# Performance work log

Hardware: AMD Instinct MI355X
Metric: run time of the kernel (lower is better)

The kernel has to match this reference:

```python
import jax, jax.numpy as jnp
import numpy as np

N, E, F, H, C, G = 100000, 1000000, 64, 64, 10, 256


def setup_inputs() -> dict:
    key = jax.random.key(0)
    ks = jax.random.split(key, 16)
    s = 1.0 / np.sqrt(F)
    sh = 1.0 / np.sqrt(H)
    return {
        "x": jax.random.normal(ks[0], (N, F), dtype=jnp.float32),
        "edge_index": jax.random.randint(ks[1], (2, E), 0, N, dtype=jnp.int32),
        "edge_attr": jax.random.uniform(ks[2], (E,), dtype=jnp.float32),
        "batch": jnp.sort(jax.random.randint(ks[3], (N,), 0, G, dtype=jnp.int32)),
        "W1r": jax.random.uniform(ks[4], (F, H), minval=-s, maxval=s),
        "W1s": jax.random.uniform(ks[5], (F, H), minval=-s, maxval=s),
        "b1": jax.random.uniform(ks[6], (H,), minval=-s, maxval=s),
        "W2r": jax.random.uniform(ks[7], (H, H), minval=-sh, maxval=sh),
        "W2s": jax.random.uniform(ks[8], (H, H), minval=-sh, maxval=sh),
        "b2": jax.random.uniform(ks[9], (H,), minval=-sh, maxval=sh),
        "W3r": jax.random.uniform(ks[10], (H, H), minval=-sh, maxval=sh),
        "W3s": jax.random.uniform(ks[11], (H, H), minval=-sh, maxval=sh),
        "b3": jax.random.uniform(ks[12], (H,), minval=-sh, maxval=sh),
        "Wl": jax.random.uniform(ks[13], (H, C), minval=-sh, maxval=sh),
        "bl": jax.random.uniform(ks[14], (C,), minval=-sh, maxval=sh),
    }


def graph_conv(x, src, dst, ew, W_rel, W_root, b):
    # gather neighbor feats, weight per-edge, scatter-add to destination
    msgs = x[src] * ew[:, None]                              # [E, F]
    agg = jax.ops.segment_sum(msgs, dst, num_segments=N)     # [N, F]
    return agg @ W_rel + x @ W_root + b                      # [N, H]


def reference(x, edge_index, edge_attr, batch,
              W1r, W1s, b1, W2r, W2s, b2, W3r, W3s, b3, Wl, bl):
    src, dst = edge_index[0], edge_index[1]
    h = jax.nn.relu(graph_conv(x, src, dst, edge_attr, W1r, W1s, b1))
    h = jax.nn.relu(graph_conv(h, src, dst, edge_attr, W2r, W2s, b2))
    h = jax.nn.relu(graph_conv(h, src, dst, edge_attr, W3r, W3s, b3))
    # global mean pool over graphs in the batch
    sums = jax.ops.segment_sum(h, batch, num_segments=G)      # [G, H]
    cnts = jax.ops.segment_sum(jnp.ones((N,), h.dtype), batch, num_segments=G)
    pooled = sums / jnp.maximum(cnts, 1.0)[:, None]
    # dropout is identity in eval mode
    return pooled @ Wl + bl                                   # [G, C]
```

## Files before the change

kernel.cpp:

```cpp
#include <hip/hip_runtime.h>


#define GCN_F 64
#define GCN_C 10
#define CB_SHIFT 9
#define CB_NODES 512
#define NCB_MAX 200
#define CAP 7168
#define SC_CHUNK 2048

typedef __attribute__((ext_vector_type(8))) short bf16x8;
typedef __attribute__((ext_vector_type(4))) float f32x4;

__device__ __forceinline__ unsigned short f2b(float v) {
    union { float f; unsigned int u; } c; c.f = v;
    unsigned int u = c.u;
    return (unsigned short)((u + 0x7FFFu + ((u >> 16) & 1u)) >> 16);
}
__device__ __forceinline__ float b2f(unsigned short u) {
    union { unsigned int u; float f; } c; c.u = ((unsigned int)u) << 16; return c.f;
}

__global__ __launch_bounds__(256) void cvtz_kernel(const float* __restrict__ in,
                                                   unsigned short* __restrict__ out,
                                                   int n4, int* __restrict__ zp, int zn) {
    int gid = blockIdx.x * 256 + threadIdx.x;
    if (gid < zn) zp[gid] = 0;
    int stride = gridDim.x * 256;
    for (int i = gid; i < n4; i += stride) {
        float4 v = reinterpret_cast<const float4*>(in)[i];
        ushort4 o;
        o.x = f2b(v.x); o.y = f2b(v.y); o.z = f2b(v.z); o.w = f2b(v.w);
        reinterpret_cast<ushort4*>(out)[i] = o;
    }
}

__global__ __launch_bounds__(256) void histC_kernel(const int* __restrict__ dst,
                                                    int* __restrict__ bcnt,
                                                    int E, int NCB) {
    __shared__ int h[NCB_MAX];
    int tid = threadIdx.x;
    for (int i = tid; i < NCB; i += 256) h[i] = 0;
    __syncthreads();
    int e0 = blockIdx.x * 4096 + tid;
#pragma unroll
    for (int k = 0; k < 16; ++k) {
        int e = e0 + k * 256;
        if (e < E) atomicAdd(&h[dst[e] >> CB_SHIFT], 1);
    }
    __syncthreads();
    for (int i = tid; i < NCB; i += 256)
        if (h[i]) atomicAdd(&bcnt[i], h[i]);
}

__global__ void bscan_kernel(const int* __restrict__ bcnt, int* __restrict__ gstart,
                             int nb) {
    int lane = threadIdx.x;
    int carry = 0;
    for (int base = 0; base < nb; base += 64) {
        int i = base + lane;
        int v = (i < nb) ? bcnt[i] : 0;
        int sc = v;
#pragma unroll
        for (int off = 1; off < 64; off <<= 1) {
            int t = __shfl_up(sc, off);
            if (lane >= off) sc += t;
        }
        if (i < nb) gstart[i] = carry + sc - v;
        carry += __shfl(sc, 63);
    }
    if (lane == 0) gstart[nb] = carry;
}

__global__ __launch_bounds__(256) void scatterC_kernel(
    const int* __restrict__ src, const int* __restrict__ dst,
    const float* __restrict__ ew, const int* __restrict__ gstart,
    int* __restrict__ gcursor, int2* __restrict__ ebufA, int E, int NCB) {
    __shared__ int2 recS[SC_CHUNK];
    __shared__ int gdest[SC_CHUNK];
    __shared__ int hist[NCB_MAX];
    __shared__ int lstart[NCB_MAX];
    __shared__ int gbase[NCB_MAX];
    __shared__ int cur[NCB_MAX];
    __shared__ int sb[256];

    int tid = threadIdx.x;
    int base = blockIdx.x * SC_CHUNK;
    int m = min(SC_CHUNK, E - base);

    for (int i = tid; i < NCB; i += 256) hist[i] = 0;
    __syncthreads();

    int2 rec[8];
    int bk[8];
#pragma unroll
    for (int k = 0; k < 8; ++k) {
        int e = base + k * 256 + tid;
        if (e < E) {
            int d = dst[e];
            bk[k] = d >> CB_SHIFT;
            rec[k] = make_int2(src[e] | ((d & (CB_NODES - 1)) << 17),
                               __float_as_int(ew[e]));
            atomicAdd(&hist[bk[k]], 1);
        } else bk[k] = -1;
    }
    __syncthreads();

    int v = (tid < NCB) ? hist[tid] : 0;
    sb[tid] = v;
    __syncthreads();
    for (int o = 1; o < 256; o <<= 1) {
        int t = (tid >= o) ? sb[tid - o] : 0;
        __syncthreads();
        sb[tid] += t;
        __syncthreads();
    }
    if (tid < NCB) {
        int excl = sb[tid] - v;
        lstart[tid] = excl;
        cur[tid] = excl;
        gbase[tid] = (v > 0) ? atomicAdd(&gcursor[tid], v) : 0;
    }
    __syncthreads();

#pragma unroll
    for (int k = 0; k < 8; ++k) {
        if (bk[k] >= 0) {
            int p = atomicAdd(&cur[bk[k]], 1);
            recS[p] = rec[k];
            gdest[p] = gstart[bk[k]] + gbase[bk[k]] + (p - lstart[bk[k]]);
        }
    }
    __syncthreads();

    for (int i = tid; i < m; i += 256) ebufA[gdest[i]] = recS[i];
}

__global__ __launch_bounds__(256) void sortCB_kernel(
    const int2* __restrict__ ebufA, const int* __restrict__ gstart,
    int2* __restrict__ ebufS, int* __restrict__ offsets, int N, int E) {
    __shared__ int2 rec[CAP];
    __shared__ int cnt[CB_NODES];
    __shared__ int cur[CB_NODES];
    __shared__ int sbuf[256];
    int cb = blockIdx.x, tid = threadIdx.x;
    int e0 = gstart[cb], e1 = gstart[cb + 1];
    int m = min(e1 - e0, CAP);

    for (int i = tid; i < m; i += 256) rec[i] = ebufA[e0 + i];
    for (int i = tid; i < CB_NODES; i += 256) cnt[i] = 0;
    __syncthreads();
    for (int i = tid; i < m; i += 256)
        atomicAdd(&cnt[(unsigned)rec[i].x >> 17], 1);
    __syncthreads();

    int c0 = cnt[2 * tid], c1 = cnt[2 * tid + 1];
    int part = c0 + c1;
    sbuf[tid] = part;
    __syncthreads();
    for (int off = 1; off < 256; off <<= 1) {
        int t = (tid >= off) ? sbuf[tid - off] : 0;
        __syncthreads();
        sbuf[tid] += t;
        __syncthreads();
    }
    int excl = sbuf[tid] - part;
    int pre0 = excl, pre1 = excl + c0;
    cur[2 * tid] = pre0;
    cur[2 * tid + 1] = pre1;
    int g0 = cb * CB_NODES + 2 * tid;
    if (g0 <= N)     offsets[g0]     = e0 + pre0;
    if (g0 + 1 <= N) offsets[g0 + 1] = e0 + pre1;
    __syncthreads();

    for (int i = tid; i < m; i += 256) {
        int d9 = (unsigned)rec[i].x >> 17;
        int pos = atomicAdd(&cur[d9], 1);
        ebufS[e0 + pos] = make_int2(rec[i].x & 0x1FFFF, rec[i].y);
    }
}

__global__ __launch_bounds__(256) void layer_kernel(
    const unsigned short* __restrict__ xin, const int* __restrict__ offsets,
    const int2* __restrict__ ebufS, const float* __restrict__ Wr,
    const float* __restrict__ Ws, const float* __restrict__ b,
    unsigned short* __restrict__ out, int n)
{
    __shared__ __align__(16) unsigned short bfrag[2][2][4][64][8];
    __shared__ __align__(16) unsigned short aggS[4][16][72];
    int tid = threadIdx.x, lane = tid & 63, wave = tid >> 6;

    for (int i = tid; i < 8192; i += 256) {
        int op = i >> 12;
        int ks = (i >> 11) & 1;
        int ct = (i >> 9) & 3;
        int l  = (i >> 3) & 63;
        int j  = i & 7;
        int k   = ks * 32 + (l >> 4) * 8 + j;
        int col = ct * 16 + (l & 15);
        const float* W = op ? Ws : Wr;
        ((unsigned short*)bfrag)[i] = f2b(W[k * GCN_F + col]);
    }
    __syncthreads();

    int l8 = lane & 7;
    int grp = lane >> 3;
    int gbase = (lane & 56) << 2;
    int wbase = blockIdx.x * 64 + wave * 16;

#pragma unroll
    for (int half = 0; half < 2; ++half) {
        int node = wbase + half * 8 + grp;
        bool nv = node < n;
        int p0 = 0, p1 = 0;
        if (nv) { p0 = offsets[node]; p1 = offsets[node + 1]; }
        float acc[8] = {0.f, 0.f, 0.f, 0.f, 0.f, 0.f, 0.f, 0.f};

        int idx = p0 + l8;
        bool v = idx < p1;
        if (__any(v)) {
            int2 er = ebufS[v ? idx : 0];
            int s  = v ? er.x : 0;
            int wb = v ? er.y : 0;

            for (int c = 1;; ++c) {
                int idxn = p0 + c * 8 + l8;
                bool vn = idxn < p1;
                int2 ern = ebufS[vn ? idxn : 0];

                int sj[8], wj[8];
#pragma unroll
                for (int j = 0; j < 8; ++j) {
                    sj[j] = __builtin_amdgcn_ds_bpermute(gbase + (j << 2), s);
                    wj[j] = __builtin_amdgcn_ds_bpermute(gbase + (j << 2), wb);
                }
                int4 r[8];
#pragma unroll
                for (int j = 0; j < 8; ++j)
                    r[j] = *reinterpret_cast<const int4*>(
                        xin + ((size_t)sj[j] << 6) + l8 * 8);
#pragma unroll
                for (int j = 0; j < 8; ++j) {
                    float wf = __int_as_float(wj[j]);
                    acc[0] = fmaf(__int_as_float(r[j].x << 16),        wf, acc[0]);
                    acc[1] = fmaf(__int_as_float(r[j].x & 0xFFFF0000), wf, acc[1]);
                    acc[2] = fmaf(__int_as_float(r[j].y << 16),        wf, acc[2]);
                    acc[3] = fmaf(__int_as_float(r[j].y & 0xFFFF0000), wf, acc[3]);
                    acc[4] = fmaf(__int_as_float(r[j].z << 16),        wf, acc[4]);
                    acc[5] = fmaf(__int_as_float(r[j].z & 0xFFFF0000), wf, acc[5]);
                    acc[6] = fmaf(__int_as_float(r[j].w << 16),        wf, acc[6]);
                    acc[7] = fmaf(__int_as_float(r[j].w & 0xFFFF0000), wf, acc[7]);
                }

                if (!__any(vn)) break;
                s  = vn ? ern.x : 0;
                wb = vn ? ern.y : 0;
            }
        }

        int4 o;
        o.x = (int)f2b(acc[0]) | ((int)f2b(acc[1]) << 16);
        o.y = (int)f2b(acc[2]) | ((int)f2b(acc[3]) << 16);
        o.z = (int)f2b(acc[4]) | ((int)f2b(acc[5]) << 16);
        o.w = (int)f2b(acc[6]) | ((int)f2b(acc[7]) << 16);
        *reinterpret_cast<int4*>(&aggS[wave][half * 8 + grp][l8 * 8]) = o;
    }

    int l15 = lane & 15, lhi = lane >> 4;

    bf16x8 B[2][2][4];
#pragma unroll
    for (int op = 0; op < 2; ++op)
#pragma unroll
        for (int ks = 0; ks < 2; ++ks)
#pragma unroll
            for (int ct = 0; ct < 4; ++ct)
                B[op][ks][ct] = *reinterpret_cast<const bf16x8*>(&bfrag[op][ks][ct][lane][0]);

    float bias[4];
#pragma unroll
    for (int ct = 0; ct < 4; ++ct) bias[ct] = b[ct * 16 + l15];

    bf16x8 a0 = *reinterpret_cast<const bf16x8*>(&aggS[wave][l15][lhi * 8]);
    bf16x8 a1 = *reinterpret_cast<const bf16x8*>(&aggS[wave][l15][32 + lhi * 8]);
    const unsigned short* xp = xin + (size_t)min(wbase + l15, n - 1) * GCN_F + lhi * 8;
    bf16x8 x0 = *reinterpret_cast<const bf16x8*>(xp);
    bf16x8 x1 = *reinterpret_cast<const bf16x8*>(xp + 32);

#pragma unroll
    for (int ct = 0; ct < 4; ++ct) {
        f32x4 acc = {0.f, 0.f, 0.f, 0.f};
        acc = __builtin_amdgcn_mfma_f32_16x16x32_bf16(a0, B[0][0][ct], acc, 0, 0, 0);
        acc = __builtin_amdgcn_mfma_f32_16x16x32_bf16(a1, B[0][1][ct], acc, 0, 0, 0);
        acc = __builtin_amdgcn_mfma_f32_16x16x32_bf16(x0, B[1][0][ct], acc, 0, 0, 0);
        acc = __builtin_amdgcn_mfma_f32_16x16x32_bf16(x1, B[1][1][ct], acc, 0, 0, 0);
        int col = ct * 16 + l15;
#pragma unroll
        for (int r = 0; r < 4; ++r) {
            int orow = wbase + lhi * 4 + r;
            if (orow < n) {
                float v = fmaxf(acc[r] + bias[ct], 0.f);
                out[(size_t)orow * GCN_F + col] = f2b(v);
            }
        }
    }
}

__global__ __launch_bounds__(256) void pool_kernel(
    const unsigned short* __restrict__ h, const int* __restrict__ batch,
    const float* __restrict__ Wl, const float* __restrict__ bl,
    float* __restrict__ out, int n)
{
    int g    = blockIdx.x;
    int tid  = threadIdx.x;
    int lane = tid & 63;
    int wave = tid >> 6;

    int i0, i1;
    {
        int lo = 0, hi = n;
        while (lo < hi) { int mid = (lo + hi) >> 1; if (batch[mid] < g) lo = mid + 1; else hi = mid; }
        i0 = lo;
        lo = i0; hi = n;
        while (lo < hi) { int mid = (lo + hi) >> 1; if (batch[mid] < g + 1) lo = mid + 1; else hi = mid; }
        i1 = lo;
    }

    float s = 0.f;
    for (int i = i0 + wave; i < i1; i += 4) s += b2f(h[(size_t)i * GCN_F + lane]);

    __shared__ float sp[4][GCN_F];
    sp[wave][lane] = s;
    __syncthreads();
    if (wave == 0) {
        float tot = sp[0][lane] + sp[1][lane] + sp[2][lane] + sp[3][lane];
        float cntf = (float)(i1 - i0);
        sp[0][lane] = tot / fmaxf(cntf, 1.f);
    }
    __syncthreads();
    if (tid < GCN_C) {
        float o = bl[tid];
#pragma unroll
        for (int j = 0; j < GCN_F; ++j) o += sp[0][j] * Wl[j * GCN_C + tid];
        out[g * GCN_C + tid] = o;
    }
}

extern "C" void kernel_launch(void* const* d_in, const int* in_sizes, int n_in,
                              void* d_out, int out_size, void* d_ws, size_t ws_size,
                              hipStream_t stream) {
    const float* x     = (const float*)d_in[0];
    const int*   ei    = (const int*)d_in[1];
    const float* ew    = (const float*)d_in[2];
    const int*   batch = (const int*)d_in[3];
    const float* W1r   = (const float*)d_in[4];
    const float* W1s   = (const float*)d_in[5];
    const float* b1    = (const float*)d_in[6];
    const float* W2r   = (const float*)d_in[7];
    const float* W2s   = (const float*)d_in[8];
    const float* b2    = (const float*)d_in[9];
    const float* W3r   = (const float*)d_in[10];
    const float* W3s   = (const float*)d_in[11];
    const float* b3    = (const float*)d_in[12];
    const float* Wl    = (const float*)d_in[13];
    const float* bl    = (const float*)d_in[14];
    float* out = (float*)d_out;

    const int N = in_sizes[0] / GCN_F;
    const int E = in_sizes[2];
    const int G = out_size / GCN_C;
    const int NCB = (N + CB_NODES - 1) / CB_NODES;

    const int* src = ei;
    const int* dst = ei + E;

    char* ws = (char*)d_ws;
    size_t off = 0;
    size_t csz = ((size_t)NCB * 4 + 15) & ~(size_t)15;
    int* bcnt    = (int*)(ws + off);  off += csz;
    int* gcursor = (int*)(ws + off);  off += csz;
    int* gstart  = (int*)(ws + off);  off += ((size_t)(NCB + 1) * 4 + 15) & ~(size_t)15;
    int* offsets = (int*)(ws + off);  off += ((size_t)(N + 1) * 4 + 15) & ~(size_t)15;
    int2* ebufA  = (int2*)(ws + off); off += (size_t)E * 8;
    int2* ebufS  = (int2*)(ws + off); off += (size_t)E * 8;
    unsigned short* buf0 = (unsigned short*)(ws + off); off += (size_t)N * GCN_F * 2;
    unsigned short* buf1 = (unsigned short*)(ws + off); off += (size_t)N * GCN_F * 2;

    int hblocks = (E + 4095) / 4096;
    int sblocks = (E + SC_CHUNK - 1) / SC_CHUNK;
    int zcount  = (int)(csz * 2 / 4);

    cvtz_kernel<<<1024, 256, 0, stream>>>(x, buf0, N * GCN_F / 4, bcnt, zcount);
    histC_kernel<<<hblocks, 256, 0, stream>>>(dst, bcnt, E, NCB);
    bscan_kernel<<<1, 64, 0, stream>>>(bcnt, gstart, NCB);
    scatterC_kernel<<<sblocks, 256, 0, stream>>>(src, dst, ew, gstart, gcursor, ebufA, E, NCB);
    sortCB_kernel<<<NCB, 256, 0, stream>>>(ebufA, gstart, ebufS, offsets, N, E);

    const int LBLK = (N + 63) / 64;
    layer_kernel<<<LBLK, 256, 0, stream>>>(buf0, offsets, ebufS, W1r, W1s, b1, buf1, N);
    layer_kernel<<<LBLK, 256, 0, stream>>>(buf1, offsets, ebufS, W2r, W2s, b2, buf0, N);
    layer_kernel<<<LBLK, 256, 0, stream>>>(buf0, offsets, ebufS, W3r, W3s, b3, buf1, N);

    pool_kernel<<<G, 256, 0, stream>>>(buf1, batch, Wl, bl, out, N);
}
```

Before: 245.3 us.

## Stage per-wave edge lists in LDS and interleave two node halves in gather

Each wave now loads its 16 nodes' offsets in one read, copies the contiguous edge records into a per-wave LDS buffer (when they fit in CAP_W entries), and then gathers features for both node halves in one interleaved loop. Edge lookups come from LDS with clamped indices and zeroed weights instead of global loads plus bpermute broadcasts. The goal is to shorten the serialized edge-load to feature-load dependency chain and keep more feature loads in flight. In exchange it adds LDS use that may reduce occupancy, runs a uniform trip count equal to the wave's longest node, and falls back to a slow serial per-edge loop when a wave has more edges than fit.

```diff
diff --git a/kernel.cpp b/kernel.cpp
--- a/kernel.cpp
+++ b/kernel.cpp
@@ -8,6 +8,7 @@
 #define NCB_MAX 200
 #define CAP 7168
 #define SC_CHUNK 2048
+#define CAP_W 384
 
 typedef __attribute__((ext_vector_type(8))) short bf16x8;
 typedef __attribute__((ext_vector_type(4))) float f32x4;
@@ -188,6 +189,7 @@
 {
     __shared__ __align__(16) unsigned short bfrag[2][2][4][64][8];
     __shared__ __align__(16) unsigned short aggS[4][16][72];
+    __shared__ __align__(16) int2 eLDS[4][CAP_W];
     int tid = threadIdx.x, lane = tid & 63, wave = tid >> 6;
 
     for (int i = tid; i < 8192; i += 256) {
@@ -201,69 +203,133 @@
         const float* W = op ? Ws : Wr;
         ((unsigned short*)bfrag)[i] = f2b(W[k * GCN_F + col]);
     }
-    __syncthreads();
 
     int l8 = lane & 7;
     int grp = lane >> 3;
-    int gbase = (lane & 56) << 2;
-    int wbase = blockIdx.x * 64 + wave * 16;
-
-#pragma unroll
-    for (int half = 0; half < 2; ++half) {
-        int node = wbase + half * 8 + grp;
-        bool nv = node < n;
-        int p0 = 0, p1 = 0;
-        if (nv) { p0 = offsets[node]; p1 = offsets[node + 1]; }
-        float acc[8] = {0.f, 0.f, 0.f, 0.f, 0.f, 0.f, 0.f, 0.f};
-
-        int idx = p0 + l8;
-        bool v = idx < p1;
-        if (__any(v)) {
-            int2 er = ebufS[v ? idx : 0];
-            int s  = v ? er.x : 0;
-            int wb = v ? er.y : 0;
-
-            for (int c = 1;; ++c) {
-                int idxn = p0 + c * 8 + l8;
-                bool vn = idxn < p1;
-                int2 ern = ebufS[vn ? idxn : 0];
-
-                int sj[8], wj[8];
+    int w0 = blockIdx.x * 64 + wave * 16;
+
+    int offl = offsets[min(w0 + min(lane, 16), n)];
+    int we0   = __builtin_amdgcn_readlane(offl, 0);
+    int off16 = __builtin_amdgcn_readlane(offl, 16);
+    int cnt = off16 - we0;
+    int p0A = __builtin_amdgcn_ds_bpermute(grp * 4, offl);
+    int p1A = __builtin_amdgcn_ds_bpermute((grp + 1) * 4, offl);
+    int p0B = __builtin_amdgcn_ds_bpermute((8 + grp) * 4, offl);
+    int p1B = __builtin_amdgcn_ds_bpermute((9 + grp) * 4, offl);
+
+    bool allstaged = (cnt <= CAP_W);
+    if (allstaged) {
+        for (int i = lane; i < cnt; i += 64) eLDS[wave][i] = ebufS[we0 + i];
+    }
+    __syncthreads();
+
+    float accA[8] = {0.f,0.f,0.f,0.f,0.f,0.f,0.f,0.f};
+    float accB[8] = {0.f,0.f,0.f,0.f,0.f,0.f,0.f,0.f};
+
+    if (cnt > 0) {
+        if (allstaged) {
+            int ebA = p0A - we0, ebB = p0B - we0;
+            int lastA = max(p1A - 1 - we0, 0);
+            int lastB = max(p1B - 1 - we0, 0);
+            int myc = max((p1A - p0A + 7) >> 3, (p1B - p0B + 7) >> 3);
+            for (int o = 1; o < 64; o <<= 1) myc = max(myc, __shfl_xor(myc, o));
+
+            for (int c = 0; c < myc; ++c) {
+                int sA[8], sB[8];
+                float wfA[8], wfB[8];
 #pragma unroll
                 for (int j = 0; j < 8; ++j) {
-                    sj[j] = __builtin_amdgcn_ds_bpermute(gbase + (j << 2), s);
-                    wj[j] = __builtin_amdgcn_ds_bpermute(gbase + (j << 2), wb);
+                    int q = min(ebA + c * 8 + j, lastA);
+                    int2 t = eLDS[wave][q];
+                    sA[j] = t.x;
+                    wfA[j] = (p0A + c * 8 + j < p1A) ? __int_as_float(t.y) : 0.f;
                 }
-                int4 r[8];
+                int4 rA[8];
 #pragma unroll
                 for (int j = 0; j < 8; ++j)
-                    r[j] = *reinterpret_cast<const int4*>(
-                        xin + ((size_t)sj[j] << 6) + l8 * 8);
+                    rA[j] = *reinterpret_cast<const int4*>(
+                        xin + ((size_t)sA[j] << 6) + l8 * 8);
 #pragma unroll
                 for (int j = 0; j < 8; ++j) {
-                    float wf = __int_as_float(wj[j]);
-                    acc[0] = fmaf(__int_as_float(r[j].x << 16),        wf, acc[0]);
-                    acc[1] = fmaf(__int_as_float(r[j].x & 0xFFFF0000), wf, acc[1]);
-                    acc[2] = fmaf(__int_as_float(r[j].y << 16),        wf, acc[2]);
-                    acc[3] = fmaf(__int_as_float(r[j].y & 0xFFFF0000), wf, acc[3]);
-                    acc[4] = fmaf(__int_as_float(r[j].z << 16),        wf, acc[4]);
-                    acc[5] = fmaf(__int_as_float(r[j].z & 0xFFFF0000), wf, acc[5]);
-                    acc[6] = fmaf(__int_as_float(r[j].w << 16),        wf, acc[6]);
-                    acc[7] = fmaf(__int_as_float(r[j].w & 0xFFFF0000), wf, acc[7]);
+                    int q = min(ebB + c * 8 + j, lastB);
+                    int2 t = eLDS[wave][q];
+                    sB[j] = t.x;
+                    wfB[j] = (p0B + c * 8 + j < p1B) ? __int_as_float(t.y) : 0.f;
                 }
-
-                if (!__any(vn)) break;
-                s  = vn ? ern.x : 0;
-                wb = vn ? ern.y : 0;
+                int4 rB[8];
+#pragma unroll
+                for (int j = 0; j < 8; ++j)
+                    rB[j] = *reinterpret_cast<const int4*>(
+                        xin + ((size_t)sB[j] << 6) + l8 * 8);
+#pragma unroll
+                for (int j = 0; j < 8; ++j) {
+                    float wf = wfA[j];
+                    accA[0] = fmaf(__int_as_float(rA[j].x << 16),        wf, accA[0]);
+                    accA[1] = fmaf(__int_as_float(rA[j].x & 0xFFFF0000), wf, accA[1]);
+                    accA[2] = fmaf(__int_as_float(rA[j].y << 16),        wf, accA[2]);
+                    accA[3] = fmaf(__int_as_float(rA[j].y & 0xFFFF0000), wf, accA[3]);
+                    accA[4] = fmaf(__int_as_float(rA[j].z << 16),        wf, accA[4]);
+                    accA[5] = fmaf(__int_as_float(rA[j].z & 0xFFFF0000), wf, accA[5]);
+                    accA[6] = fmaf(__int_as_float(rA[j].w << 16),        wf, accA[6]);
+                    accA[7] = fmaf(__int_as_float(rA[j].w & 0xFFFF0000), wf, accA[7]);
+                }
+#pragma unroll
+                for (int j = 0; j < 8; ++j) {
+                    float wf = wfB[j];
+                    accB[0] = fmaf(__int_as_float(rB[j].x << 16),        wf, accB[0]);
+                    accB[1] = fmaf(__int_as_float(rB[j].x & 0xFFFF0000), wf, accB[1]);
+                    accB[2] = fmaf(__int_as_float(rB[j].y << 16),        wf, accB[2]);
+                    accB[3] = fmaf(__int_as_float(rB[j].y & 0xFFFF0000), wf, accB[3]);
+                    accB[4] = fmaf(__int_as_float(rB[j].z << 16),        wf, accB[4]);
+                    accB[5] = fmaf(__int_as_float(rB[j].z & 0xFFFF0000), wf, accB[5]);
+                    accB[6] = fmaf(__int_as_float(rB[j].w << 16),        wf, accB[6]);
+                    accB[7] = fmaf(__int_as_float(rB[j].w & 0xFFFF0000), wf, accB[7]);
+                }
+            }
+        } else {
+            for (int e = p0A; e < p1A; ++e) {
+                int2 er = ebufS[e];
+                float wf = __int_as_float(er.y);
+                const int4 r = *reinterpret_cast<const int4*>(
+                    xin + ((size_t)er.x << 6) + l8 * 8);
+                accA[0] = fmaf(__int_as_float(r.x << 16),        wf, accA[0]);
+                accA[1] = fmaf(__int_as_float(r.x & 0xFFFF0000), wf, accA[1]);
+                accA[2] = fmaf(__int_as_float(r.y << 16),        wf, accA[2]);
+                accA[3] = fmaf(__int_as_float(r.y & 0xFFFF0000), wf, accA[3]);
+                accA[4] = fmaf(__int_as_float(r.z << 16),        wf, accA[4]);
+                accA[5] = fmaf(__int_as_float(r.z & 0xFFFF0000), wf, accA[5]);
+                accA[6] = fmaf(__int_as_float(r.w << 16),        wf, accA[6]);
+                accA[7] = fmaf(__int_as_float(r.w & 0xFFFF0000), wf, accA[7]);
+            }
+            for (int e = p0B; e < p1B; ++e) {
+                int2 er = ebufS[e];
+                float wf = __int_as_float(er.y);
+                const int4 r = *reinterpret_cast<const int4*>(
+                    xin + ((size_t)er.x << 6) + l8 * 8);
+                accB[0] = fmaf(__int_as_float(r.x << 16),        wf, accB[0]);
+                accB[1] = fmaf(__int_as_float(r.x & 0xFFFF0000), wf, accB[1]);
+                accB[2] = fmaf(__int_as_float(r.y << 16),        wf, accB[2]);
+                accB[3] = fmaf(__int_as_float(r.y & 0xFFFF0000), wf, accB[3]);
+                accB[4] = fmaf(__int_as_float(r.z << 16),        wf, accB[4]);
+                accB[5] = fmaf(__int_as_float(r.z & 0xFFFF0000), wf, accB[5]);
+                accB[6] = fmaf(__int_as_float(r.w << 16),        wf, accB[6]);
+                accB[7] = fmaf(__int_as_float(r.w & 0xFFFF0000), wf, accB[7]);
             }
         }
-
+    }
+
+    {
         int4 o;
-        o.x = (int)f2b(acc[0]) | ((int)f2b(acc[1]) << 16);
-        o.y = (int)f2b(acc[2]) | ((int)f2b(acc[3]) << 16);
-        o.z = (int)f2b(acc[4]) | ((int)f2b(acc[5]) << 16);
-        o.w = (int)f2b(acc[6]) | ((int)f2b(acc[7]) << 16);
-        *reinterpret_cast<int4*>(&aggS[wave][half * 8 + grp][l8 * 8]) = o;
+        o.x = (int)f2b(accA[0]) | ((int)f2b(accA[1]) << 16);
+        o.y = (int)f2b(accA[2]) | ((int)f2b(accA[3]) << 16);
+        o.z = (int)f2b(accA[4]) | ((int)f2b(accA[5]) << 16);
+        o.w = (int)f2b(accA[6]) | ((int)f2b(accA[7]) << 16);
+        *reinterpret_cast<int4*>(&aggS[wave][grp][l8 * 8]) = o;
+        o.x = (int)f2b(accB[0]) | ((int)f2b(accB[1]) << 16);
+        o.y = (int)f2b(accB[2]) | ((int)f2b(accB[3]) << 16);
+        o.z = (int)f2b(accB[4]) | ((int)f2b(accB[5]) << 16);
+        o.w = (int)f2b(accB[6]) | ((int)f2b(accB[7]) << 16);
+        *reinterpret_cast<int4*>(&aggS[wave][8 + grp][l8 * 8]) = o;
     }
 
     int l15 = lane & 15, lhi = lane >> 4;
@@ -283,7 +349,7 @@
 
     bf16x8 a0 = *reinterpret_cast<const bf16x8*>(&aggS[wave][l15][lhi * 8]);
     bf16x8 a1 = *reinterpret_cast<const bf16x8*>(&aggS[wave][l15][32 + lhi * 8]);
-    const unsigned short* xp = xin + (size_t)min(wbase + l15, n - 1) * GCN_F + lhi * 8;
+    const unsigned short* xp = xin + (size_t)min(w0 + l15, n - 1) * GCN_F + lhi * 8;
     bf16x8 x0 = *reinterpret_cast<const bf16x8*>(xp);
     bf16x8 x1 = *reinterpret_cast<const bf16x8*>(xp + 32);
 
@@ -297,7 +363,7 @@
         int col = ct * 16 + l15;
 #pragma unroll
         for (int r = 0; r < 4; ++r) {
-            int orow = wbase + lhi * 4 + r;
+            int orow = w0 + lhi * 4 + r;
             if (orow < n) {
                 float v = fmaxf(acc[r] + bias[ct], 0.f);
                 out[(size_t)orow * GCN_F + col] = f2b(v);
```

Measured after the change: 263.6 us. 1.07x slower.
